# Optimization experiments

Measured on AMD Instinct MI355X. Metric: run time of the kernel, lower is better.

## Reference

```python
import jax, jax.numpy as jnp
import numpy as np

B, T, C, HS = 4, 4096, 1024, 64

def setup_inputs() -> dict:
    key = jax.random.key(0)
    kx, kq, kk, kv = jax.random.split(key, 4)
    x = jax.random.normal(kx, (B, T, C), dtype=jnp.float32)
    s = 1.0 / np.sqrt(C)
    Wq = jax.random.normal(kq, (C, HS), dtype=jnp.float32) * s
    Wk = jax.random.normal(kk, (C, HS), dtype=jnp.float32) * s
    Wv = jax.random.normal(kv, (C, HS), dtype=jnp.float32) * s
    return {"x": x, "Wq": Wq, "Wk": Wk, "Wv": Wv}

def reference(x, Wq, Wk, Wv):
    # q,k,v: [B,T,HS]
    q = jnp.einsum('btc,ch->bth', x, Wq)
    k = jnp.einsum('btc,ch,->bth', x, Wk) if False else jnp.einsum('btc,ch->bth', x, Wk)
    v = jnp.einsum('btc,ch->bth', x, Wv)
    dk = q.shape[-1]
    wei = jnp.einsum('bth,bsh->bts', q, k) * (dk ** -0.5)  # [B,T,T]
    Tq = wei.shape[1]
    causal = jnp.tril(jnp.ones((Tq, Tq), dtype=bool))
    wei = jnp.where(causal, wei, -jnp.inf)
    wei = jax.nn.softmax(wei, axis=-1)
    out = jnp.einsum('bts,bsh->bth', wei, v)  # [B,T,HS]
    return out
```

## Files before the change

kernel.cpp:

```cpp
#include <hip/hip_runtime.h>
#include <stdint.h>

typedef __attribute__((ext_vector_type(8))) short short8v;
typedef __attribute__((ext_vector_type(4))) float float4v;

__device__ __forceinline__ unsigned short f32_to_bf16(float f) {
    union { float f; uint32_t u; } v; v.f = f;
    uint32_t u = v.u;
    u += 0x7FFFu + ((u >> 16) & 1u);
    return (unsigned short)(u >> 16);
}

#define T_LEN 4096
#define C_DIM 1024
#define HSZ 64

__global__ void wt_kernel(const float* __restrict__ Wq, const float* __restrict__ Wk,
                          const float* __restrict__ Wv, unsigned short* __restrict__ Wtp) {
    int idx = blockIdx.x * blockDim.x + threadIdx.x;
    int e    = idx & 7;
    int lane = (idx >> 3) & 63;
    int ks   = (idx >> 9) & 31;
    int ct   = idx >> 14;
    int g = lane >> 4, c = lane & 15;
    int k   = ks * 32 + g * 8 + e;
    int col = (ct & 3) * 16 + c;
    int m   = ct >> 2;
    const float* W = (m == 0) ? Wq : ((m == 1) ? Wk : Wv);
    Wtp[idx] = f32_to_bf16(W[(size_t)k * 64 + col]);
}

#define XLD 1032

__global__ __launch_bounds__(256) void qkv_kernel(
    const float* __restrict__ x, const unsigned short* __restrict__ Wtp,
    unsigned short* __restrict__ qo, unsigned short* __restrict__ kp,
    unsigned short* __restrict__ vp)
{
    __shared__ __align__(16) unsigned short xs[16 * XLD];
    const int tid = threadIdx.x;
    const int bid = (int)blockIdx.x;
    const int rowidx = (((bid >> 1) & 3) << 8) + ((bid >> 3) << 1) + (bid & 1);
    const int row0 = rowidx * 16;

    #pragma unroll
    for (int i = 0; i < 16; ++i) {
        int f   = i * 256 + tid;
        int row = f >> 8, c4 = f & 255;
        const float4 val = *((const float4*)x + (size_t)(row0 + row) * 256 + c4);
        union { unsigned short s[4]; uint64_t u; } pk;
        pk.s[0] = f32_to_bf16(val.x); pk.s[1] = f32_to_bf16(val.y);
        pk.s[2] = f32_to_bf16(val.z); pk.s[3] = f32_to_bf16(val.w);
        *(uint64_t*)(&xs[row * XLD + c4 * 4]) = pk.u;
    }
    __syncthreads();

    const int wave = tid >> 6, lane = tid & 63;
    const int g = lane >> 4, c = lane & 15;

    float4v acc0 = {0,0,0,0}, acc1 = {0,0,0,0}, acc2 = {0,0,0,0};
    const unsigned short* wp0 = Wtp + (size_t)((wave * 3 + 0) * 32) * 512 + lane * 8;
    const unsigned short* wp1 = Wtp + (size_t)((wave * 3 + 1) * 32) * 512 + lane * 8;
    const unsigned short* wp2 = Wtp + (size_t)((wave * 3 + 2) * 32) * 512 + lane * 8;
    #pragma unroll 4
    for (int ks = 0; ks < 32; ++ks) {
        const int koff = ks * 32 + g * 8;
        short8v a  = *(const short8v*)(&xs[c * XLD + koff]);
        short8v b0 = *(const short8v*)(wp0 + ks * 512);
        short8v b1 = *(const short8v*)(wp1 + ks * 512);
        short8v b2 = *(const short8v*)(wp2 + ks * 512);
        acc0 = __builtin_amdgcn_mfma_f32_16x16x32_bf16(a, b0, acc0, 0, 0, 0);
        acc1 = __builtin_amdgcn_mfma_f32_16x16x32_bf16(a, b1, acc1, 0, 0, 0);
        acc2 = __builtin_amdgcn_mfma_f32_16x16x32_bf16(a, b2, acc2, 0, 0, 0);
    }

    float4v accs[3] = {acc0, acc1, acc2};
    #pragma unroll
    for (int t = 0; t < 3; ++t) {
        int ct = wave * 3 + t;
        int m = ct >> 2, hcol = (ct & 3) * 16 + c;
        if (m == 2) {
            const int r0 = row0 + g * 4;
            const int b  = r0 >> 12;
            const int s0_ = r0 & 4095;
            const int t2h = s0_ >> 5;
            const int gv  = (s0_ >> 3) & 3;
            const int e0  = s0_ & 7;
            union { unsigned short s[4]; uint64_t u; } pk;
            #pragma unroll
            for (int j = 0; j < 4; ++j) pk.s[j] = f32_to_bf16(accs[t][j]);
            *(uint64_t*)(vp + (size_t)b * 262144 + t2h * 2048 + (ct & 3) * 512
                            + (gv * 16 + c) * 8 + e0) = pk.u;
        } else if (m == 1) {
            const int fbase = ((row0 & 4095) >> 6) * 8 + (((row0 & 4095) >> 4) & 3) * 2 + (hcol >> 5);
            const int b = row0 >> 12;
            unsigned short* kb = kp + (size_t)b * 262144 + (size_t)fbase * 512
                                 + (((hcol >> 3) & 3) * 16) * 8 + (hcol & 7);
            #pragma unroll
            for (int j = 0; j < 4; ++j)
                kb[(g * 4 + j) * 8] = f32_to_bf16(accs[t][j]);
        } else {
            float sc = 0.125f;
            #pragma unroll
            for (int j = 0; j < 4; ++j)
                qo[(size_t)(row0 + g * 4 + j) * 64 + hcol] = f32_to_bf16(accs[t][j] * sc);
        }
    }
}

#define PLD 72

__global__ __launch_bounds__(512) void attn_kernel(
    const unsigned short* __restrict__ qi, const unsigned short* __restrict__ kp,
    const unsigned short* __restrict__ vp, float* __restrict__ out)
{
    __shared__ __align__(16) unsigned short Ps[8][16 * PLD];
    __shared__ float CombO[6][16][64];
    __shared__ float CombM[6][16];
    __shared__ float CombL[6][16];

    const int tid   = threadIdx.x;
    const int wave  = tid >> 6, lane = tid & 63;
    const int qh    = wave & 1, slice = wave >> 1;
    const int g = lane >> 4, c = lane & 15;

    const int bid   = (int)blockIdx.x;
    const int batch = (bid >> 1) & 3;
    const int q0    = bid & 1;
    const int m_    = bid >> 3;
    const int mm    = m_ & 31;
    const int qb = q0 ? ((m_ < 32) ? 2 * mm + 1 : 126 - 2 * mm)
                      : ((m_ < 32) ? 2 * mm     : 127 - 2 * mm);

    const int rbase = qb * 32 + qh * 16;
    const size_t bo  = (size_t)batch * T_LEN * HSZ;
    const size_t bov = (size_t)batch * 262144;

    short8v qf0 = *(const short8v*)(qi + bo + (size_t)(rbase + c) * 64 +  0 + g * 8);
    short8v qf1 = *(const short8v*)(qi + bo + (size_t)(rbase + c) * 64 + 32 + g * 8);

    float4v acc[4];
    #pragma unroll
    for (int i2 = 0; i2 < 4; ++i2) acc[i2] = (float4v){0,0,0,0};
    float mrow = -3e38f;
    float lsum = 0.f;

    const int nt_w = ((rbase + 15) >> 6) + 1;
    unsigned short* Pw = &Ps[wave][0];

    short8v kf[8], kn[8];

    auto TILE = [&](int t, const short8v* kb) {
        const int s0 = t * 64;

        float4v sa[4];
        #pragma unroll
        for (int ct = 0; ct < 4; ++ct) {
            float4v z = {0, 0, 0, 0};
            z = __builtin_amdgcn_mfma_f32_16x16x32_bf16(kb[ct * 2 + 0], qf0, z, 0, 0, 0);
            sa[ct] = __builtin_amdgcn_mfma_f32_16x16x32_bf16(kb[ct * 2 + 1], qf1, z, 0, 0, 0);
        }

        short8v vf0[4];
        #pragma unroll
        for (int dt = 0; dt < 4; ++dt)
            vf0[dt] = *(const short8v*)(vp + bov + (size_t)(t * 8 + dt) * 512 + lane * 8);

        if (s0 + 63 > rbase) {
            #pragma unroll
            for (int ct = 0; ct < 4; ++ct)
                #pragma unroll
                for (int j = 0; j < 4; ++j)
                    if (s0 + ct * 16 + g * 4 + j > rbase + c) sa[ct][j] = -3e38f;
        }

        float mx01 = fmaxf(fmaxf(sa[0][0], sa[0][1]), fmaxf(sa[0][2], sa[0][3]));
        float mx11 = fmaxf(fmaxf(sa[1][0], sa[1][1]), fmaxf(sa[1][2], sa[1][3]));
        float mx21 = fmaxf(fmaxf(sa[2][0], sa[2][1]), fmaxf(sa[2][2], sa[2][3]));
        float mx31 = fmaxf(fmaxf(sa[3][0], sa[3][1]), fmaxf(sa[3][2], sa[3][3]));
        float mx = fmaxf(fmaxf(mx01, mx11), fmaxf(mx21, mx31));
        mx = fmaxf(mx, __shfl_xor(mx, 16, 64));
        mx = fmaxf(mx, __shfl_xor(mx, 32, 64));
        const float nm = fmaxf(mrow, mx);
        const float al = __expf(mrow - nm);
        mrow = nm;
        float ps = 0.f;
        #pragma unroll
        for (int ct = 0; ct < 4; ++ct)
            #pragma unroll
            for (int j = 0; j < 4; ++j) {
                float p = __expf(sa[ct][j] - nm);
                sa[ct][j] = p;
                ps += p;
            }
        lsum = lsum * al + ps;
        #pragma unroll
        for (int dt = 0; dt < 4; ++dt)
            #pragma unroll
            for (int j = 0; j < 4; ++j) acc[dt][j] *= al;

        #pragma unroll
        for (int ct = 0; ct < 4; ++ct) {
            union { unsigned short s[4]; uint64_t u; } pk4;
            #pragma unroll
            for (int j = 0; j < 4; ++j) pk4.s[j] = f32_to_bf16(sa[ct][j]);
            *(uint64_t*)(&Pw[c * PLD + ct * 16 + g * 4]) = pk4.u;
        }

        short8v vf1[4];
        #pragma unroll
        for (int dt = 0; dt < 4; ++dt)
            vf1[dt] = *(const short8v*)(vp + bov + (size_t)(t * 8 + 4 + dt) * 512 + lane * 8);

        short8v pa0 = *(const short8v*)(&Pw[c * PLD +  0 + g * 8]);
        short8v pa1 = *(const short8v*)(&Pw[c * PLD + 32 + g * 8]);

        #pragma unroll
        for (int dt = 0; dt < 4; ++dt)
            acc[dt] = __builtin_amdgcn_mfma_f32_16x16x32_bf16(vf0[dt], pa0, acc[dt], 0, 0, 0);
        #pragma unroll
        for (int dt = 0; dt < 4; ++dt)
            acc[dt] = __builtin_amdgcn_mfma_f32_16x16x32_bf16(vf1[dt], pa1, acc[dt], 0, 0, 0);
    };

    auto LOADK = [&](int t, short8v* kd) {
        #pragma unroll
        for (int f = 0; f < 8; ++f)
            kd[f] = *(const short8v*)(kp + bov + (size_t)(t * 8 + f) * 512 + lane * 8);
    };

    int t = slice;
    if (t < nt_w) {
        LOADK(t, kf);
        while (true) {
            const bool h1 = (t + 4 < nt_w);
            if (h1) LOADK(t + 4, kn);
            TILE(t, kf);
            if (!h1) break;
            t += 4;
            const bool h2 = (t + 4 < nt_w);
            if (h2) LOADK(t + 4, kf);
            TILE(t, kn);
            if (!h2) break;
            t += 4;
        }
    }

    lsum += __shfl_xor(lsum, 16, 64);
    lsum += __shfl_xor(lsum, 32, 64);

    if (slice > 0) {
        const int sidx = (slice - 1) * 2 + qh;
        #pragma unroll
        for (int dt = 0; dt < 4; ++dt)
            #pragma unroll
            for (int j = 0; j < 4; ++j)
                CombO[sidx][c][dt * 16 + g * 4 + j] = acc[dt][j];
        if (g == 0) {
            CombM[sidx][c] = mrow;
            CombL[sidx][c] = lsum;
        }
    }
    __syncthreads();

    if (slice == 0) {
        float M = mrow;
        #pragma unroll
        for (int s = 0; s < 3; ++s) M = fmaxf(M, CombM[s * 2 + qh][c]);
        const float a0 = __expf(mrow - M);
        float as[3];
        float lt = lsum * a0;
        #pragma unroll
        for (int s = 0; s < 3; ++s) {
            as[s] = __expf(CombM[s * 2 + qh][c] - M);
            lt += as[s] * CombL[s * 2 + qh][c];
        }
        const float linv = 1.0f / lt;
        #pragma unroll
        for (int dt = 0; dt < 4; ++dt) {
            float4 o;
            float* op = &o.x;
            #pragma unroll
            for (int j = 0; j < 4; ++j) {
                float v = acc[dt][j] * a0;
                #pragma unroll
                for (int s = 0; s < 3; ++s)
                    v += as[s] * CombO[s * 2 + qh][c][dt * 16 + g * 4 + j];
                op[j] = v * linv;
            }
            *(float4*)(out + bo + (size_t)(rbase + c) * 64 + dt * 16 + g * 4) = o;
        }
    }
}

extern "C" void kernel_launch(void* const* d_in, const int* in_sizes, int n_in,
                              void* d_out, int out_size, void* d_ws, size_t ws_size,
                              hipStream_t stream) {
    const float* x  = (const float*)d_in[0];
    const float* Wq = (const float*)d_in[1];
    const float* Wk = (const float*)d_in[2];
    const float* Wv = (const float*)d_in[3];

    unsigned short* Wt = (unsigned short*)d_ws;
    unsigned short* q  = (unsigned short*)((char*)d_ws + (size_t)3 * 65536 * 2);
    unsigned short* kp = q + (size_t)4 * T_LEN * HSZ;
    unsigned short* vp = kp + (size_t)4 * T_LEN * HSZ;
    float* out = (float*)d_out;

    hipLaunchKernelGGL(wt_kernel,  dim3(768), dim3(256), 0, stream, Wq, Wk, Wv, Wt);
    hipLaunchKernelGGL(qkv_kernel, dim3(1024), dim3(256), 0, stream, x, Wt, q, kp, vp);
    hipLaunchKernelGGL(attn_kernel, dim3(512), dim3(512), 0, stream, q, kp, vp, out);
}
```

Measured before the change: 59.08 us.

## Double-buffer x chunks in QKV projection to overlap loads with MFMA

The QKV projection kernel now stages x in four 256-column chunks across two small LDS buffers instead of loading the whole 16x1024 row tile up front. The next chunk's global loads are issued into registers before the MFMA loop on the current chunk, then converted and written to the other buffer. This aims to hide global load latency behind compute and to cut LDS use, which may allow more blocks per CU. The cost is two extra barriers per chunk and more registers held for the prefetched data.

```diff
diff --git a/kernel.cpp b/kernel.cpp
--- a/kernel.cpp
+++ b/kernel.cpp
@@ -30,48 +30,74 @@
     Wtp[idx] = f32_to_bf16(W[(size_t)k * 64 + col]);
 }
 
-#define XLD 1032
+#define XCH 264
 
 __global__ __launch_bounds__(256) void qkv_kernel(
     const float* __restrict__ x, const unsigned short* __restrict__ Wtp,
     unsigned short* __restrict__ qo, unsigned short* __restrict__ kp,
     unsigned short* __restrict__ vp)
 {
-    __shared__ __align__(16) unsigned short xs[16 * XLD];
+    __shared__ __align__(16) unsigned short xs2[2][16 * XCH];
     const int tid = threadIdx.x;
     const int bid = (int)blockIdx.x;
     const int rowidx = (((bid >> 1) & 3) << 8) + ((bid >> 3) << 1) + (bid & 1);
     const int row0 = rowidx * 16;
 
-    #pragma unroll
-    for (int i = 0; i < 16; ++i) {
-        int f   = i * 256 + tid;
-        int row = f >> 8, c4 = f & 255;
-        const float4 val = *((const float4*)x + (size_t)(row0 + row) * 256 + c4);
-        union { unsigned short s[4]; uint64_t u; } pk;
-        pk.s[0] = f32_to_bf16(val.x); pk.s[1] = f32_to_bf16(val.y);
-        pk.s[2] = f32_to_bf16(val.z); pk.s[3] = f32_to_bf16(val.w);
-        *(uint64_t*)(&xs[row * XLD + c4 * 4]) = pk.u;
-    }
-    __syncthreads();
-
     const int wave = tid >> 6, lane = tid & 63;
     const int g = lane >> 4, c = lane & 15;
+
+    const int lrow = tid >> 6;
+    float4 ld[4];
+
+    auto LOADX = [&](int cs) {
+        #pragma unroll
+        for (int i = 0; i < 4; ++i) {
+            int f = i * 256 + tid;
+            int row = f >> 6, c4 = f & 63;
+            ld[i] = *((const float4*)x + (size_t)(row0 + row) * 256 + cs * 64 + c4);
+        }
+    };
+    auto WRITEX = [&](int buf) {
+        #pragma unroll
+        for (int i = 0; i < 4; ++i) {
+            int f = i * 256 + tid;
+            int row = f >> 6, c4 = f & 63;
+            union { unsigned short s[4]; uint64_t u; } pk;
+            pk.s[0] = f32_to_bf16(ld[i].x); pk.s[1] = f32_to_bf16(ld[i].y);
+            pk.s[2] = f32_to_bf16(ld[i].z); pk.s[3] = f32_to_bf16(ld[i].w);
+            *(uint64_t*)(&xs2[buf][row * XCH + c4 * 4]) = pk.u;
+        }
+    };
+    (void)lrow;
+
+    LOADX(0);
+    WRITEX(0);
+    __syncthreads();
 
     float4v acc0 = {0,0,0,0}, acc1 = {0,0,0,0}, acc2 = {0,0,0,0};
     const unsigned short* wp0 = Wtp + (size_t)((wave * 3 + 0) * 32) * 512 + lane * 8;
     const unsigned short* wp1 = Wtp + (size_t)((wave * 3 + 1) * 32) * 512 + lane * 8;
     const unsigned short* wp2 = Wtp + (size_t)((wave * 3 + 2) * 32) * 512 + lane * 8;
-    #pragma unroll 4
-    for (int ks = 0; ks < 32; ++ks) {
-        const int koff = ks * 32 + g * 8;
-        short8v a  = *(const short8v*)(&xs[c * XLD + koff]);
-        short8v b0 = *(const short8v*)(wp0 + ks * 512);
-        short8v b1 = *(const short8v*)(wp1 + ks * 512);
-        short8v b2 = *(const short8v*)(wp2 + ks * 512);
-        acc0 = __builtin_amdgcn_mfma_f32_16x16x32_bf16(a, b0, acc0, 0, 0, 0);
-        acc1 = __builtin_amdgcn_mfma_f32_16x16x32_bf16(a, b1, acc1, 0, 0, 0);
-        acc2 = __builtin_amdgcn_mfma_f32_16x16x32_bf16(a, b2, acc2, 0, 0, 0);
+
+    for (int cs = 0; cs < 4; ++cs) {
+        if (cs < 3) LOADX(cs + 1);
+        const int buf = cs & 1;
+        #pragma unroll
+        for (int k8 = 0; k8 < 8; ++k8) {
+            const int ks = cs * 8 + k8;
+            short8v a  = *(const short8v*)(&xs2[buf][c * XCH + k8 * 32 + g * 8]);
+            short8v b0 = *(const short8v*)(wp0 + ks * 512);
+            short8v b1 = *(const short8v*)(wp1 + ks * 512);
+            short8v b2 = *(const short8v*)(wp2 + ks * 512);
+            acc0 = __builtin_amdgcn_mfma_f32_16x16x32_bf16(a, b0, acc0, 0, 0, 0);
+            acc1 = __builtin_amdgcn_mfma_f32_16x16x32_bf16(a, b1, acc1, 0, 0, 0);
+            acc2 = __builtin_amdgcn_mfma_f32_16x16x32_bf16(a, b2, acc2, 0, 0, 0);
+        }
+        if (cs < 3) {
+            __syncthreads();
+            WRITEX(buf ^ 1);
+            __syncthreads();
+        }
     }
 
     float4v accs[3] = {acc0, acc1, acc2};
```

Measured after the change: 57.83 us. 1.02x faster.
